# Optimization experiments

Measured on AMD Instinct MI355X. Metric: run time of the kernel, lower is better.

The kernel has to match this reference:

```python
import jax, jax.numpy as jnp
import numpy as np

N_HEADS = 32
N_KV = 16
HEAD_DIM = 128
REPEATS = N_HEADS // N_KV
ROPE_THETA = 10000.0
SOFTCAP = 50.0
SCALE = 1.0 / np.sqrt(144.0)


def _rope_cos_sin(L, dtype):
    half = HEAD_DIM // 2
    inv_freq = 1.0 / (ROPE_THETA ** (jnp.arange(0, HEAD_DIM, 2, dtype=jnp.float32) / HEAD_DIM))
    ang = jnp.arange(L, dtype=jnp.float32)[:, None] * inv_freq[None, :]  # [L, half]
    return jnp.cos(ang).astype(dtype), jnp.sin(ang).astype(dtype)


def _apply_rope(t, cos, sin):
    # t: [B, H, L, D]; non-traditional (rotate-half) RoPE
    half = HEAD_DIM // 2
    t1, t2 = t[..., :half], t[..., half:]
    c = cos[None, None, :, :]
    s = sin[None, None, :, :]
    return jnp.concatenate([t1 * c - t2 * s, t2 * c + t1 * s], axis=-1)


def setup_inputs() -> dict:
    key = jax.random.key(0)
    k1, k2, k3, k4, k5 = jax.random.split(key, 5)
    B, L, D = 1, 2048, 4608
    x = jax.random.normal(k1, (B, L, D), dtype=jnp.float32)
    wq = jax.random.normal(k2, (N_HEADS * HEAD_DIM, D), dtype=jnp.float32) * 0.02
    wk = jax.random.normal(k3, (N_KV * HEAD_DIM, D), dtype=jnp.float32) * 0.02
    wv = jax.random.normal(k4, (N_KV * HEAD_DIM, D), dtype=jnp.float32) * 0.02
    wo = jax.random.normal(k5, (D, N_HEADS * HEAD_DIM), dtype=jnp.float32) * 0.02
    mask = jnp.tril(jnp.ones((L, L), dtype=bool))  # causal
    return {"x": x, "mask": mask, "wq": wq, "wk": wk, "wv": wv, "wo": wo}


def reference(x, mask, wq, wk, wv, wo):
    B, L, D = x.shape
    q = (x @ wq.T).reshape(B, L, N_HEADS, HEAD_DIM).transpose(0, 2, 1, 3)
    k = (x @ wk.T).reshape(B, L, N_KV, HEAD_DIM).transpose(0, 2, 1, 3)
    v = (x @ wv.T).reshape(B, L, N_KV, HEAD_DIM).transpose(0, 2, 1, 3)

    cos, sin = _rope_cos_sin(L, x.dtype)
    q = _apply_rope(q, cos, sin) * jnp.asarray(SCALE, x.dtype)
    k = _apply_rope(k, cos, sin)

    # GQA: group queries per kv head -> [B, n_kv, repeats, L, D]
    qg = q.reshape(B, N_KV, REPEATS, L, HEAD_DIM)
    scores = jnp.einsum("bgrqd,bgkd->bgrqk", qg, k)
    scores = jnp.tanh(scores / SOFTCAP) * SOFTCAP
    neg = jnp.asarray(jnp.finfo(scores.dtype).min, scores.dtype)
    scores = jnp.where(mask[None, None, None, :, :], scores, neg)
    probs = jax.nn.softmax(scores, axis=-1)
    out = jnp.einsum("bgrqk,bgkd->bgrqd", probs, v)  # [B, n_kv, rep, L, D]
    out = out.reshape(B, N_HEADS, L, HEAD_DIM).transpose(0, 2, 1, 3).reshape(B, L, -1)
    return out @ wo.T
```

## Files before the change

### kernel.cpp

```cpp
#include <hip/hip_runtime.h>
#include <hip/hip_bf16.h>
#include <math.h>

typedef unsigned short u16;
typedef __attribute__((ext_vector_type(8))) short s16x8;
typedef __attribute__((ext_vector_type(4))) float f32x4;

#define SCALE 0.083333333333333329f
#define LDO 4128

__device__ __forceinline__ u16 f2bf(float f) {
    unsigned u = __float_as_uint(f);
    unsigned r = 0x7fffu + ((u >> 16) & 1u);
    return (u16)((u + r) >> 16);
}
__device__ __forceinline__ float bf2f(u16 v) {
    return __uint_as_float(((unsigned)v) << 16);
}

__global__ __launch_bounds__(256) void cast_kernel(const float* __restrict__ in,
                                                   u16* __restrict__ out) {
    size_t i = ((size_t)blockIdx.x * 256 + threadIdx.x) * 4;
    float4 v = *(const float4*)(in + i);
    ushort4 o;
    o.x = f2bf(v.x); o.y = f2bf(v.y); o.z = f2bf(v.z); o.w = f2bf(v.w);
    *(ushort4*)(out + i) = o;
}

__global__ __launch_bounds__(256) void cast_pad_kernel(const float* __restrict__ in,
                                                       u16* __restrict__ out) {
    size_t i = ((size_t)blockIdx.x * 256 + threadIdx.x) * 4;
    size_t row = i >> 12;
    int col = (int)(i & 4095);
    float4 v = *(const float4*)(in + i);
    ushort4 o;
    o.x = f2bf(v.x); o.y = f2bf(v.y); o.z = f2bf(v.z); o.w = f2bf(v.w);
    *(ushort4*)(out + row * LDO + col) = o;
}

__global__ __launch_bounds__(256) void rope_table_kernel(float* __restrict__ cosT,
                                                         float* __restrict__ sinT) {
    int idx = blockIdx.x * 256 + threadIdx.x;
    int i = idx & 63, pos = idx >> 6;
    float inv = __expf(-((float)i / 64.0f) * 9.210340371976184f);
    float ang = (float)pos * inv;
    cosT[idx] = cosf(ang);
    sinT[idx] = sinf(ang);
}

__global__ __launch_bounds__(256) void rope_q_kernel(const u16* __restrict__ T16,
                                                     u16* __restrict__ Qb,
                                                     const float* __restrict__ cosT,
                                                     const float* __restrict__ sinT) {
    int idx = blockIdx.x * 256 + threadIdx.x;
    int i4 = (idx & 15) << 2;
    int head = (idx >> 4) & 31;
    int pos = idx >> 9;
    size_t rbase = (size_t)pos * 8192 + head * 128 + i4;
    ushort4 t1v = *(const ushort4*)&T16[rbase];
    ushort4 t2v = *(const ushort4*)&T16[rbase + 64];
    float4 cv = *(const float4*)&cosT[(pos << 6) + i4];
    float4 sv = *(const float4*)&sinT[(pos << 6) + i4];
    ushort4 o1, o2;
    {
        float t1 = bf2f(t1v.x), t2 = bf2f(t2v.x);
        o1.x = f2bf((t1 * cv.x - t2 * sv.x) * SCALE);
        o2.x = f2bf((t2 * cv.x + t1 * sv.x) * SCALE);
    }
    {
        float t1 = bf2f(t1v.y), t2 = bf2f(t2v.y);
        o1.y = f2bf((t1 * cv.y - t2 * sv.y) * SCALE);
        o2.y = f2bf((t2 * cv.y + t1 * sv.y) * SCALE);
    }
    {
        float t1 = bf2f(t1v.z), t2 = bf2f(t2v.z);
        o1.z = f2bf((t1 * cv.z - t2 * sv.z) * SCALE);
        o2.z = f2bf((t2 * cv.z + t1 * sv.z) * SCALE);
    }
    {
        float t1 = bf2f(t1v.w), t2 = bf2f(t2v.w);
        o1.w = f2bf((t1 * cv.w - t2 * sv.w) * SCALE);
        o2.w = f2bf((t2 * cv.w + t1 * sv.w) * SCALE);
    }
    size_t wbase = (size_t)pos * 4096 + head * 128 + i4;
    *(ushort4*)&Qb[wbase]      = o1;
    *(ushort4*)&Qb[wbase + 64] = o2;
}

__global__ __launch_bounds__(256) void rope_k_kernel(const u16* __restrict__ T16,
                                                     u16* __restrict__ Kb,
                                                     const float* __restrict__ cosT,
                                                     const float* __restrict__ sinT) {
    int idx = blockIdx.x * 256 + threadIdx.x;
    int i4 = (idx & 15) << 2;
    int head = (idx >> 4) & 15;
    int pos = idx >> 8;
    size_t rbase = (size_t)pos * 8192 + 4096 + head * 128 + i4;
    ushort4 t1v = *(const ushort4*)&T16[rbase];
    ushort4 t2v = *(const ushort4*)&T16[rbase + 64];
    float4 cv = *(const float4*)&cosT[(pos << 6) + i4];
    float4 sv = *(const float4*)&sinT[(pos << 6) + i4];
    ushort4 o1, o2;
    {
        float t1 = bf2f(t1v.x), t2 = bf2f(t2v.x);
        o1.x = f2bf(t1 * cv.x - t2 * sv.x);
        o2.x = f2bf(t2 * cv.x + t1 * sv.x);
    }
    {
        float t1 = bf2f(t1v.y), t2 = bf2f(t2v.y);
        o1.y = f2bf(t1 * cv.y - t2 * sv.y);
        o2.y = f2bf(t2 * cv.y + t1 * sv.y);
    }
    {
        float t1 = bf2f(t1v.z), t2 = bf2f(t2v.z);
        o1.z = f2bf(t1 * cv.z - t2 * sv.z);
        o2.z = f2bf(t2 * cv.z + t1 * sv.z);
    }
    {
        float t1 = bf2f(t1v.w), t2 = bf2f(t2v.w);
        o1.w = f2bf(t1 * cv.w - t2 * sv.w);
        o2.w = f2bf(t2 * cv.w + t1 * sv.w);
    }
    size_t wbase = (size_t)pos * 2048 + head * 128 + i4;
    *(ushort4*)&Kb[wbase]      = o1;
    *(ushort4*)&Kb[wbase + 64] = o2;
}

__global__ __launch_bounds__(256) void vtrans_kernel(const u16* __restrict__ T16,
                                                     u16* __restrict__ Vt) {
    __shared__ u16 tile[64][65];
    int bc = (blockIdx.x & 31) << 6;
    int bl = (blockIdx.x >> 5) << 6;
    int tx = threadIdx.x & 15, ty = threadIdx.x >> 4;
    #pragma unroll
    for (int rr = 0; rr < 4; rr++) {
        int row = rr * 16 + ty;
        ushort4 v = *(const ushort4*)&T16[(size_t)(bl + row) * 8192 + 6144 + bc + tx * 4];
        tile[row][tx * 4 + 0] = v.x;
        tile[row][tx * 4 + 1] = v.y;
        tile[row][tx * 4 + 2] = v.z;
        tile[row][tx * 4 + 3] = v.w;
    }
    __syncthreads();
    #pragma unroll
    for (int cc = 0; cc < 4; cc++) {
        int col = cc * 16 + ty;
        int l0 = tx * 4;
        ushort4 g;
        g.x = tile[l0 + 0][col];
        g.y = tile[l0 + 1][col];
        g.z = tile[l0 + 2][col];
        g.w = tile[l0 + 3][col];
        *(ushort4*)&Vt[(size_t)(bc + col) * 2048 + bl + l0] = g;
    }
}

#define STAGE_A(buf, ktt, l)                                                            \
    __builtin_amdgcn_global_load_lds(                                                   \
        (const __attribute__((address_space(1))) unsigned int*)(aSrc + (size_t)(ktt) * 64 + (size_t)(l) * 64 * lda), \
        (__attribute__((address_space(3))) unsigned int*)(&lds[buf][0][(l) * 4096 + ldsoff]), 16, 0, 0)
#define STAGE_B(buf, ktt, l)                                                            \
    __builtin_amdgcn_global_load_lds(                                                   \
        (const __attribute__((address_space(1))) unsigned int*)(bSrc + (size_t)(ktt) * 64 + (size_t)(l) * 64 * ldb), \
        (__attribute__((address_space(3))) unsigned int*)(&lds[buf][1][(l) * 4096 + ldsoff]), 16, 0, 0)

template<bool OUT_BF16>
__device__ __forceinline__ void gemm256_core(const u16* __restrict__ A,
                                             const u16* __restrict__ B,
                                             void* __restrict__ C,
                                             int N, int K, int lda, int ldb,
                                             int bm, int bn,
                                             u16 (&lds)[2][2][16384]) {
    int t = threadIdx.x;
    int lane = t & 63, wave = t >> 6;
    int wm = wave >> 2, wn = wave & 3;
    int fr = lane & 15, fq = lane >> 4;
    int sw = (fr & 7) << 4;

    int srow = wave * 8 + (lane >> 3);
    int scb = ((lane & 7) * 16) ^ (((lane >> 3) & 7) << 4);
    const u16* aSrc = A + (size_t)(bm * 256 + srow) * lda + (scb >> 1);
    const u16* bSrc = B + (size_t)(bn * 256 + srow) * ldb + (scb >> 1);
    int ldsoff = wave * 512;

    f32x4 acc[8][4];
    #pragma unroll
    for (int m = 0; m < 8; m++)
        #pragma unroll
        for (int n = 0; n < 4; n++)
            acc[m][n] = (f32x4){0.f, 0.f, 0.f, 0.f};

    STAGE_B(0, 0, 0); STAGE_B(0, 0, 1); STAGE_B(0, 0, 2); STAGE_B(0, 0, 3);
    STAGE_A(0, 0, 0); STAGE_A(0, 0, 1); STAGE_A(0, 0, 2); STAGE_A(0, 0, 3);

    int nt = K >> 6;
    for (int it = 0; it < nt; ++it) {
        int cur = it & 1, nxt = cur ^ 1;
        bool more = (it + 1 < nt);
        const char* Ab = (const char*)&lds[cur][0][0];
        const char* Bb = (const char*)&lds[cur][1][0];
        int cb0 = (fq * 16) ^ sw;
        int cb1 = (64 + fq * 16) ^ sw;

        if (more) {
            STAGE_B(nxt, it + 1, 0); STAGE_B(nxt, it + 1, 1);
            __builtin_amdgcn_sched_barrier(0);
            asm volatile("s_waitcnt vmcnt(2)" ::: "memory");
        } else {
            asm volatile("s_waitcnt vmcnt(0)" ::: "memory");
        }
        __builtin_amdgcn_s_barrier();
        s16x8 b0[4], a0[4];
        #pragma unroll
        for (int n = 0; n < 4; ++n)
            b0[n] = *(const s16x8*)(Bb + (wn * 64 + n * 16 + fr) * 128 + cb0);
        #pragma unroll
        for (int m = 0; m < 4; ++m)
            a0[m] = *(const s16x8*)(Ab + (wm * 128 + m * 16 + fr) * 128 + cb0);
        __builtin_amdgcn_s_setprio(1);
        #pragma unroll
        for (int m = 0; m < 4; ++m)
            #pragma unroll
            for (int n = 0; n < 4; ++n)
                acc[m][n] = __builtin_amdgcn_mfma_f32_16x16x32_bf16(a0[m], b0[n], acc[m][n], 0, 0, 0);
        __builtin_amdgcn_s_setprio(0);
        s16x8 a1[4];
        #pragma unroll
        for (int m = 0; m < 4; ++m)
            a1[m] = *(const s16x8*)(Ab + (wm * 128 + (4 + m) * 16 + fr) * 128 + cb0);
        __builtin_amdgcn_s_barrier();

        if (more) { STAGE_B(nxt, it + 1, 2); STAGE_B(nxt, it + 1, 3); }
        __builtin_amdgcn_s_setprio(1);
        #pragma unroll
        for (int m = 0; m < 4; ++m)
            #pragma unroll
            for (int n = 0; n < 4; ++n)
                acc[4 + m][n] = __builtin_amdgcn_mfma_f32_16x16x32_bf16(a1[m], b0[n], acc[4 + m][n], 0, 0, 0);
        __builtin_amdgcn_s_setprio(0);
        s16x8 b1[4], a2[4];
        #pragma unroll
        for (int n = 0; n < 4; ++n)
            b1[n] = *(const s16x8*)(Bb + (wn * 64 + n * 16 + fr) * 128 + cb1);
        #pragma unroll
        for (int m = 0; m < 4; ++m)
            a2[m] = *(const s16x8*)(Ab + (wm * 128 + m * 16 + fr) * 128 + cb1);
        __builtin_amdgcn_s_barrier();

        if (more) {
            STAGE_A(nxt, it + 1, 0); STAGE_A(nxt, it + 1, 1);
            STAGE_A(nxt, it + 1, 2); STAGE_A(nxt, it + 1, 3);
        }
        __builtin_amdgcn_s_setprio(1);
        #pragma unroll
        for (int m = 0; m < 4; ++m)
            #pragma unroll
            for (int n = 0; n < 4; ++n)
                acc[m][n] = __builtin_amdgcn_mfma_f32_16x16x32_bf16(a2[m], b1[n], acc[m][n], 0, 0, 0);
        __builtin_amdgcn_s_setprio(0);
        s16x8 a3[4];
        #pragma unroll
        for (int m = 0; m < 4; ++m)
            a3[m] = *(const s16x8*)(Ab + (wm * 128 + (4 + m) * 16 + fr) * 128 + cb1);
        __builtin_amdgcn_s_barrier();

        __builtin_amdgcn_s_setprio(1);
        #pragma unroll
        for (int m = 0; m < 4; ++m)
            #pragma unroll
            for (int n = 0; n < 4; ++n)
                acc[4 + m][n] = __builtin_amdgcn_mfma_f32_16x16x32_bf16(a3[m], b1[n], acc[4 + m][n], 0, 0, 0);
        __builtin_amdgcn_s_setprio(0);
        __builtin_amdgcn_s_barrier();
    }

    #pragma unroll
    for (int m = 0; m < 8; ++m) {
        int row = bm * 256 + wm * 128 + m * 16 + fq * 4;
        #pragma unroll
        for (int n = 0; n < 4; ++n) {
            int col = bn * 256 + wn * 64 + n * 16 + fr;
            #pragma unroll
            for (int r = 0; r < 4; ++r) {
                if (OUT_BF16) ((u16*)C)[(size_t)(row + r) * N + col] = f2bf(acc[m][n][r]);
                else          ((float*)C)[(size_t)(row + r) * N + col] = acc[m][n][r];
            }
        }
    }
}

__global__ __launch_bounds__(512) void gemm256_qkv(const u16* __restrict__ A,
                                                   const u16* __restrict__ B,
                                                   u16* __restrict__ C, int K) {
    __shared__ u16 lds[2][2][16384];
    int bid = blockIdx.x;
    int x = bid & 7, j = bid >> 3;
    int bn = x * 4 + (j & 3);
    int bm = j >> 2;
    gemm256_core<true>(A, B, C, 8192, K, K, K, bm, bn, lds);
}

__global__ __launch_bounds__(512) void gemm256_out(const u16* __restrict__ A,
                                                   const u16* __restrict__ B,
                                                   float* __restrict__ C, int K) {
    __shared__ u16 lds[2][2][16384];
    int bid = blockIdx.x;
    int j = (bid & 7) * 18 + (bid >> 3);
    int bm = j & 7;
    int bn = j >> 3;
    gemm256_core<false>(A, B, C, 4608, K, LDO, LDO, bm, bn, lds);
}

__global__ __launch_bounds__(256) void attn_kernel(const u16* __restrict__ Qb,
                                                   const u16* __restrict__ Kb,
                                                   const u16* __restrict__ Vt,
                                                   u16* __restrict__ Ob) {
    __shared__ u16 Ks[64 * 128];
    __shared__ u16 Vs[128 * 64];
    __shared__ u16 Pst[4 * 1024];

    int bid = blockIdx.x;
    int hq = bid & 31;
    int qb = 31 - (bid >> 5);
    int g = hq >> 1;
    int t = threadIdx.x;
    int lane = t & 63, wave = t >> 6;
    int fr = lane & 15, fq = lane >> 4;
    int sw = (fr & 7) << 4;
    int qrow0 = qb * 64 + wave * 16;
    u16* Pw = &Pst[wave * 1024];

    s16x8 qf[4];
    #pragma unroll
    for (int s = 0; s < 4; s++)
        qf[s] = *(const s16x8*)&Qb[(size_t)(qrow0 + fr) * 4096 + hq * 128 + s * 32 + fq * 8];

    f32x4 o[8];
    #pragma unroll
    for (int c = 0; c < 8; c++) o[c] = (f32x4){0.f, 0.f, 0.f, 0.f};
    float liacc[4] = {0.f, 0.f, 0.f, 0.f};

    int w4 = wave * 4;
    int nT = qb + 1;
    for (int kt = 0; kt < nT; kt++) {
        int kv0 = kt << 6;
        __syncthreads();
        #pragma unroll
        for (int i = 0; i < 4; i++) {
            int li_ = w4 + i;
            int rk = li_ * 4 + (lane >> 4);
            int cbk = ((lane & 15) * 16) ^ ((rk & 7) << 4);
            const u16* srcK = Kb + (size_t)(kv0 + rk) * 2048 + g * 128 + (cbk >> 1);
            __builtin_amdgcn_global_load_lds(
                (const __attribute__((address_space(1))) unsigned int*)srcK,
                (__attribute__((address_space(3))) unsigned int*)(Ks + li_ * 512), 16, 0, 0);
            int rv = li_ * 8 + (lane >> 3);
            int cbv = ((lane & 7) * 16) ^ ((rv & 7) << 4);
            const u16* srcV = Vt + (size_t)(g * 128 + rv) * 2048 + kv0 + (cbv >> 1);
            __builtin_amdgcn_global_load_lds(
                (const __attribute__((address_space(1))) unsigned int*)srcV,
                (__attribute__((address_space(3))) unsigned int*)(Vs + li_ * 512), 16, 0, 0);
        }
        __syncthreads();

        if (kv0 <= qrow0 + 15) {
            f32x4 sf[4];
            #pragma unroll
            for (int j = 0; j < 4; j++) sf[j] = (f32x4){0.f, 0.f, 0.f, 0.f};
            #pragma unroll
            for (int j = 0; j < 4; j++)
                #pragma unroll
                for (int s = 0; s < 4; s++) {
                    s16x8 kf = *(const s16x8*)&Ks[(j * 16 + fr) * 128 + (((s * 64 + fq * 16) ^ sw) >> 1)];
                    sf[j] = __builtin_amdgcn_mfma_f32_16x16x32_bf16(qf[s], kf, sf[j], 0, 0, 0);
                }
            #pragma unroll
            for (int j = 0; j < 4; j++)
                #pragma unroll
                for (int r = 0; r < 4; r++) {
                    float s_ = sf[j][r];
                    float e = __builtin_amdgcn_exp2f(s_ * 0.05770780163f);
                    float p = __builtin_amdgcn_exp2f(-144.2695041f * __builtin_amdgcn_rcpf(e + 1.0f));
                    int colk = kv0 + j * 16 + fr;
                    int rowq = qrow0 + fq * 4 + r;
                    p = (colk > rowq) ? 0.0f : p;
                    sf[j][r] = p;
                    liacc[r] += p;
                }
            #pragma unroll
            for (int j = 0; j < 4; j++)
                #pragma unroll
                for (int r = 0; r < 4; r++) {
                    int row = fq * 4 + r, col = j * 16 + fr;
                    int byteoff = (row * 128 + col * 2) ^ ((row & 7) << 4);
                    *(u16*)((char*)Pw + byteoff) = f2bf(sf[j][r]);
                }
            #pragma unroll
            for (int s = 0; s < 2; s++) {
                int rbyte = (fr * 128 + s * 64 + fq * 16) ^ sw;
                s16x8 pf = *(const s16x8*)((const char*)Pw + rbyte);
                #pragma unroll
                for (int c = 0; c < 8; c++) {
                    s16x8 vf = *(const s16x8*)&Vs[(c * 16 + fr) * 64 + (((s * 64 + fq * 16) ^ sw) >> 1)];
                    o[c] = __builtin_amdgcn_mfma_f32_16x16x32_bf16(pf, vf, o[c], 0, 0, 0);
                }
            }
        }
    }
    #pragma unroll
    for (int d = 1; d < 16; d <<= 1)
        #pragma unroll
        for (int r = 0; r < 4; r++)
            liacc[r] += __shfl_xor(liacc[r], d);
    float rli[4];
    #pragma unroll
    for (int r = 0; r < 4; r++) rli[r] = __builtin_amdgcn_rcpf(liacc[r]);
    #pragma unroll
    for (int c = 0; c < 8; c++)
        #pragma unroll
        for (int r = 0; r < 4; r++) {
            int rowq = qrow0 + fq * 4 + r;
            Ob[(size_t)rowq * LDO + hq * 128 + c * 16 + fr] = f2bf(o[c][r] * rli[r]);
        }
}

extern "C" void kernel_launch(void* const* d_in, const int* in_sizes, int n_in,
                              void* d_out, int out_size, void* d_ws, size_t ws_size,
                              hipStream_t stream) {
    const float* x  = (const float*)d_in[0];
    const float* wq = (const float*)d_in[2];
    const float* wk = (const float*)d_in[3];
    const float* wv = (const float*)d_in[4];
    const float* wo = (const float*)d_in[5];
    float* out = (float*)d_out;

    char* w = (char*)d_ws;
    u16*   xb   = (u16*)(w);
    u16*   wb   = (u16*)(w + 18874368);
    u16*   T16  = (u16*)(w + 94371840);
    u16*   Ob   = (u16*)(w + 127926272);
    u16*   Qbuf = (u16*)(w + 144834560);
    u16*   Kbuf = (u16*)(w + 161611776);
    u16*   Vt   = (u16*)(w + 170000384);
    float* cosT = (float*)(w + 178388992);
    float* sinT = (float*)(w + 178913280);

    rope_table_kernel<<<512, 256, 0, stream>>>(cosT, sinT);
    cast_kernel<<<9216, 256, 0, stream>>>(x, xb);

    cast_kernel<<<18432, 256, 0, stream>>>(wq, wb);
    cast_kernel<<<9216, 256, 0, stream>>>(wk, wb + (size_t)4096 * 4608);
    cast_kernel<<<9216, 256, 0, stream>>>(wv, wb + (size_t)6144 * 4608);

    gemm256_qkv<<<256, 512, 0, stream>>>(xb, wb, T16, 4608);

    rope_q_kernel<<<4096, 256, 0, stream>>>(T16, Qbuf, cosT, sinT);
    rope_k_kernel<<<2048, 256, 0, stream>>>(T16, Kbuf, cosT, sinT);
    vtrans_kernel<<<1024, 256, 0, stream>>>(T16, Vt);

    attn_kernel<<<1024, 256, 0, stream>>>(Qbuf, Kbuf, Vt, Ob);

    cast_pad_kernel<<<18432, 256, 0, stream>>>(wo, wb);
    gemm256_out<<<144, 512, 0, stream>>>(Ob, wb, out, 4096);
}
```

Measured before the change: 394.8 us.

## Replace 256x256 output GEMM with 128x128-tile kernel to fill all CUs

Swaps the output projection GEMM from 256x256 tiles (144 blocks) to a new 128x128-tile kernel launched with 576 blocks of 256 threads. The kernel streams A and B into double-buffered LDS with direct global-to-LDS loads, XOR swizzling and MFMA 16x16x32 bf16. The aim is to fix CU under-utilisation, since 144 blocks leave many of the GPU's compute units idle. The cost is lower arithmetic intensity per tile and more global and L2 traffic.

```diff
diff --git a/kernel.cpp b/kernel.cpp
--- a/kernel.cpp
+++ b/kernel.cpp
@@ -300,15 +300,109 @@
     gemm256_core<true>(A, B, C, 8192, K, K, K, bm, bn, lds);
 }
 
-__global__ __launch_bounds__(512) void gemm256_out(const u16* __restrict__ A,
+#define OSTG_A(buf, ktt, l)                                                             \
+    __builtin_amdgcn_global_load_lds(                                                   \
+        (const __attribute__((address_space(1))) unsigned int*)(aSrc + (size_t)(ktt) * 64 + (size_t)(l) * 32 * LDO), \
+        (__attribute__((address_space(3))) unsigned int*)(&lds[buf][0][(l) * 2048 + ldsoff]), 16, 0, 0)
+#define OSTG_B(buf, ktt, l)                                                             \
+    __builtin_amdgcn_global_load_lds(                                                   \
+        (const __attribute__((address_space(1))) unsigned int*)(bSrc + (size_t)(ktt) * 64 + (size_t)(l) * 32 * LDO), \
+        (__attribute__((address_space(3))) unsigned int*)(&lds[buf][1][(l) * 2048 + ldsoff]), 16, 0, 0)
+
+__global__ __launch_bounds__(256) void gemm_out128(const u16* __restrict__ A,
                                                    const u16* __restrict__ B,
                                                    float* __restrict__ C, int K) {
-    __shared__ u16 lds[2][2][16384];
+    __shared__ u16 lds[2][2][8192];
     int bid = blockIdx.x;
-    int j = (bid & 7) * 18 + (bid >> 3);
-    int bm = j & 7;
-    int bn = j >> 3;
-    gemm256_core<false>(A, B, C, 4608, K, LDO, LDO, bm, bn, lds);
+    int j = (bid & 7) * 72 + (bid >> 3);
+    int bm = j & 15;
+    int bn = j >> 4;
+    int t = threadIdx.x;
+    int lane = t & 63, wave = t >> 6;
+    int wm = wave >> 1, wn = wave & 1;
+    int fr = lane & 15, fq = lane >> 4;
+    int sw = (fr & 7) << 4;
+
+    int srow = wave * 8 + (lane >> 3);
+    int scb = ((lane & 7) * 16) ^ (((lane >> 3) & 7) << 4);
+    const u16* aSrc = A + (size_t)(bm * 128 + srow) * LDO + (scb >> 1);
+    const u16* bSrc = B + (size_t)(bn * 128 + srow) * LDO + (scb >> 1);
+    int ldsoff = wave * 512;
+
+    f32x4 acc[4][4];
+    #pragma unroll
+    for (int m = 0; m < 4; m++)
+        #pragma unroll
+        for (int n = 0; n < 4; n++)
+            acc[m][n] = (f32x4){0.f, 0.f, 0.f, 0.f};
+
+    OSTG_B(0, 0, 0); OSTG_B(0, 0, 1); OSTG_B(0, 0, 2); OSTG_B(0, 0, 3);
+    OSTG_A(0, 0, 0); OSTG_A(0, 0, 1); OSTG_A(0, 0, 2); OSTG_A(0, 0, 3);
+
+    int nt = K >> 6;
+    for (int it = 0; it < nt; ++it) {
+        int cur = it & 1, nxt = cur ^ 1;
+        bool more = (it + 1 < nt);
+        const char* Ab = (const char*)&lds[cur][0][0];
+        const char* Bb = (const char*)&lds[cur][1][0];
+        int cb0 = (fq * 16) ^ sw;
+        int cb1 = (64 + fq * 16) ^ sw;
+
+        if (more) {
+            OSTG_B(nxt, it + 1, 0); OSTG_B(nxt, it + 1, 1);
+            OSTG_B(nxt, it + 1, 2); OSTG_B(nxt, it + 1, 3);
+            OSTG_A(nxt, it + 1, 0); OSTG_A(nxt, it + 1, 1);
+            OSTG_A(nxt, it + 1, 2); OSTG_A(nxt, it + 1, 3);
+            __builtin_amdgcn_sched_barrier(0);
+            asm volatile("s_waitcnt vmcnt(8)" ::: "memory");
+        } else {
+            asm volatile("s_waitcnt vmcnt(0)" ::: "memory");
+        }
+        __builtin_amdgcn_s_barrier();
+        s16x8 b0[4], a0[4];
+        #pragma unroll
+        for (int n = 0; n < 4; ++n)
+            b0[n] = *(const s16x8*)(Bb + (wn * 64 + n * 16 + fr) * 128 + cb0);
+        #pragma unroll
+        for (int m = 0; m < 4; ++m)
+            a0[m] = *(const s16x8*)(Ab + (wm * 64 + m * 16 + fr) * 128 + cb0);
+        __builtin_amdgcn_s_setprio(1);
+        #pragma unroll
+        for (int m = 0; m < 4; ++m)
+            #pragma unroll
+            for (int n = 0; n < 4; ++n)
+                acc[m][n] = __builtin_amdgcn_mfma_f32_16x16x32_bf16(a0[m], b0[n], acc[m][n], 0, 0, 0);
+        __builtin_amdgcn_s_setprio(0);
+        s16x8 b1[4], a1[4];
+        #pragma unroll
+        for (int n = 0; n < 4; ++n)
+            b1[n] = *(const s16x8*)(Bb + (wn * 64 + n * 16 + fr) * 128 + cb1);
+        #pragma unroll
+        for (int m = 0; m < 4; ++m)
+            a1[m] = *(const s16x8*)(Ab + (wm * 64 + m * 16 + fr) * 128 + cb1);
+        __builtin_amdgcn_s_barrier();
+
+        __builtin_amdgcn_s_setprio(1);
+        #pragma unroll
+        for (int m = 0; m < 4; ++m)
+            #pragma unroll
+            for (int n = 0; n < 4; ++n)
+                acc[m][n] = __builtin_amdgcn_mfma_f32_16x16x32_bf16(a1[m], b1[n], acc[m][n], 0, 0, 0);
+        __builtin_amdgcn_s_setprio(0);
+        __builtin_amdgcn_s_barrier();
+    }
+
+    #pragma unroll
+    for (int m = 0; m < 4; ++m) {
+        int row = bm * 128 + wm * 64 + m * 16 + fq * 4;
+        #pragma unroll
+        for (int n = 0; n < 4; ++n) {
+            int col = bn * 128 + wn * 64 + n * 16 + fr;
+            #pragma unroll
+            for (int r = 0; r < 4; ++r)
+                C[(size_t)(row + r) * 4608 + col] = acc[m][n][r];
+        }
+    }
 }
 
 __global__ __launch_bounds__(256) void attn_kernel(const u16* __restrict__ Qb,
@@ -461,5 +555,5 @@
     attn_kernel<<<1024, 256, 0, stream>>>(Qbuf, Kbuf, Vt, Ob);
 
     cast_pad_kernel<<<18432, 256, 0, stream>>>(wo, wb);
-    gemm256_out<<<144, 512, 0, stream>>>(Ob, wb, out, 4096);
-}
+    gemm_out128<<<576, 256, 0, stream>>>(Ob, wb, out, 4096);
+}
```

New measurement: 411.0 us. 1.04x slower.
